# Performance work log

Measured on AMD Instinct MI355X. Metric: run time of the kernel, lower is better.

The kernel has to match this reference:

```python
import jax, jax.numpy as jnp
import numpy as np

B, L, A = 256, 512, 40          # proteins, residues per protein, atoms per drug
FD, FT, LD = 78, 54, 128        # drug feat, protein feat, latent dim
P = L + 1                       # residues + 1 appended drug super-node


def setup_inputs() -> dict:
    key = jax.random.key(0)
    ks = iter(jax.random.split(key, 48))
    Nd = B * A
    # drug graphs: chain bonds, both directions
    i = np.arange(A - 1)
    s = np.concatenate([i, i + 1]); d = np.concatenate([i + 1, i])
    off = (np.arange(B) * A)[:, None]
    drug_ei = jnp.asarray(np.stack([(s[None] + off).ravel(), (d[None] + off).ravel()]), jnp.int32)
    drug_batch = jnp.asarray(np.repeat(np.arange(B), A), jnp.int32)
    # protein graphs: residue chain + drug super-node (local idx L) connected to all residues in order
    r = np.arange(L - 1)
    ps = np.concatenate([r, r + 1, np.full(L, L), np.arange(L)])
    pd = np.concatenate([r + 1, r, np.arange(L), np.full(L, L)])
    poff = (np.arange(B) * P)[:, None]
    prot_ei = jnp.asarray(np.stack([(ps[None] + poff).ravel(), (pd[None] + poff).ravel()]), jnp.int32)
    prot_batch = jnp.asarray(np.repeat(np.arange(B), P), jnp.int32)
    E2 = B * (2 * (L - 1) + 2 * L)

    def lin(fi, fo):
        return jax.random.normal(next(ks), (fi, fo), jnp.float32) / np.float32(np.sqrt(fi))

    def vec(fo):
        return jnp.zeros((fo,), jnp.float32)

    return dict(
        drug_x=jax.random.normal(next(ks), (Nd, FD), jnp.float32),
        drug_ei=drug_ei, drug_batch=drug_batch,
        prot_x=jax.random.normal(next(ks), (B * P, FT), jnp.float32),
        prot_ei=prot_ei, prot_batch=prot_batch,
        prot_ea=jax.random.uniform(next(ks), (E2,), jnp.float32),
        W_c1d=lin(FD, FD), b_c1d=vec(FD),
        W_c2d=lin(FD, 2 * FD), b_c2d=vec(2 * FD),
        W_rd_g=lin(2 * FD, 2 * FD), b_rd_g=vec(2 * FD), W_rd_l=lin(2 * FD, 2 * FD),
        W_fg1d=lin(2 * FD, 1024), b_fg1d=vec(1024),
        W_fg2d=lin(1024, FT), b_fg2d=vec(FT),
        W_fg3d=lin(FT, 2 * LD), b_fg3d=vec(2 * LD),
        W_att1=lin(FT, FT), b_att1=vec(FT),
        W_att2=lin(FT, 1), b_att2=vec(1),
        W_c1t=lin(FT, LD), b_c1t=vec(LD),
        W_c2t=lin(LD, 2 * LD), b_c2t=vec(2 * LD),
        W_rt_g=lin(2 * LD, 2 * LD), b_rt_g=vec(2 * LD), W_rt_l=lin(2 * LD, 2 * LD),
        W_fg1t=lin(2 * LD, 1024), b_fg1t=vec(1024),
        W_fg2t=lin(1024, 2 * LD), b_fg2t=vec(2 * LD),
        W_fc1=lin(4 * LD, 1024), b_fc1=vec(1024),
        W_fc2=lin(1024, 512), b_fc2=vec(512),
        W_out=lin(512, 1), b_out=vec(1),
    )


def _gcn(x, W, b, src, dst, ew, n):
    # PyG GCNConv: symmetric norm with self-loops (fill value 1), optional edge weights
    h = x @ W
    deg = jax.ops.segment_sum(ew, dst, num_segments=n) + 1.0
    dinv = jax.lax.rsqrt(deg)
    norm = dinv[src] * ew * dinv[dst]
    agg = jax.ops.segment_sum(h[src] * norm[:, None], dst, num_segments=n)
    return agg + h * (dinv * dinv)[:, None] + b


def _rblock(x, Wg, bg, Wl, src, dst, ew, n):
    h = jax.nn.relu(_gcn(x, Wg, bg, src, dst, ew, n))
    return jax.nn.relu(h @ Wl + x)


def reference(drug_x, drug_ei, drug_batch, prot_x, prot_ei, prot_batch, prot_ea,
              W_c1d, b_c1d, W_c2d, b_c2d, W_rd_g, b_rd_g, W_rd_l,
              W_fg1d, b_fg1d, W_fg2d, b_fg2d, W_fg3d, b_fg3d,
              W_att1, b_att1, W_att2, b_att2,
              W_c1t, b_c1t, W_c2t, b_c2t, W_rt_g, b_rt_g, W_rt_l,
              W_fg1t, b_fg1t, W_fg2t, b_fg2t,
              W_fc1, b_fc1, W_fc2, b_fc2, W_out, b_out):
    relu = jax.nn.relu
    Nd, N2 = drug_x.shape[0], prot_x.shape[0]
    sd, dd = drug_ei[0], drug_ei[1]
    ewd = jnp.ones(sd.shape[0], drug_x.dtype)
    x = relu(_gcn(drug_x, W_c1d, b_c1d, sd, dd, ewd, Nd))
    x = relu(_gcn(x, W_c2d, b_c2d, sd, dd, ewd, Nd))
    for _ in range(4):  # shared-weight residual block applied num_rblock times
        x = _rblock(x, W_rd_g, b_rd_g, W_rd_l, sd, dd, ewd, Nd)
    xg = jax.ops.segment_max(x, drug_batch, num_segments=B)  # global max pool
    x = relu(xg @ W_fg1d + b_fg1d)
    x = x @ W_fg2d + b_fg2d                                   # [B, FT]
    x_chg = relu(x @ W_fg3d + b_fg3d)                          # [B, 2*LD]
    # vectorized per-protein attention (replaces the python loop over prot_lens)
    res = prot_x.reshape(B, P, FT)[:, :L]                      # residues only
    att = jnp.tanh(res @ W_att1 + b_att1) @ W_att2 + b_att2    # [B, L, 1]
    att = jax.nn.softmax(att[..., 0], axis=1)                  # [B, L]
    att_node = jnp.concatenate([att, jnp.zeros((B, 1), att.dtype)], 1).reshape(-1)
    drug_idx = (jnp.arange(B) + 1) * P - 1
    is_drug = jnp.zeros((N2,), bool).at[drug_idx].set(True)
    st, dt = prot_ei[0], prot_ei[1]
    # edges touching a drug super-node get that residue's attention weight
    ea = jnp.where(is_drug[st], att_node[dt], jnp.where(is_drug[dt], att_node[st], prot_ea))
    x2 = prot_x.at[drug_idx].set(x)                            # inject drug embeddings
    x2 = relu(_gcn(x2, W_c1t, b_c1t, st, dt, ea, N2))
    x2 = relu(_gcn(x2, W_c2t, b_c2t, st, dt, ea, N2))
    ew1 = jnp.ones(st.shape[0], x2.dtype)
    for _ in range(4):
        x2 = _rblock(x2, W_rt_g, b_rt_g, W_rt_l, st, dt, ew1, N2)
    x2r = x2.reshape(B, P, 2 * LD)
    x2g = x2r[:, :L].max(axis=1)                               # gmp over residues (drug node masked out)
    drug_after = x2r[:, L]
    x2v = relu(x2g @ W_fg1t + b_fg1t) @ W_fg2t + b_fg2t
    xm = jnp.maximum(drug_after, x_chg)                        # max_pool1d(kernel=2) over the pair
    xc = jnp.concatenate([xm, x2v], 1)
    xc = relu(xc @ W_fc1 + b_fc1)
    xc = relu(xc @ W_fc2 + b_fc2)
    return xc @ W_out + b_out
```

## Files before the change

### kernel.cpp

```cpp
#include <hip/hip_runtime.h>
#include <cstdio>

#define B_   256
#define L_   512
#define A_   40
#define FD_  78
#define FT_  54
#define LD_  128
#define P_   513
#define ND_  (B_*A_)
#define N2_  (B_*P_)
#define EB_  2046

typedef __attribute__((ext_vector_type(8))) short short8;
typedef __attribute__((ext_vector_type(4))) float floatx4;
typedef unsigned short u16;

__device__ __forceinline__ short f2bf(float f) {
    union { float f; unsigned u; } v; v.f = f;
    unsigned u = v.u;
    u += 0x7fff + ((u >> 16) & 1);
    return (short)(u >> 16);
}
__device__ __forceinline__ float bf2f(u16 s) {
    union { unsigned u; float f; } v; v.u = ((unsigned)s) << 16; return v.f;
}

#define TBK 32
#define LDK 40
#define CSP 260

#define SYNC_LDS asm volatile("s_waitcnt lgkmcnt(0)\n\ts_barrier" ::: "memory")

__global__ __launch_bounds__(256) void gemm_mfma_k(
    const float* __restrict__ A, const short* __restrict__ WT,
    float* __restrict__ C, int M, int N, int K, int Kp)
{
    __shared__ short As[128 * LDK];
    __shared__ short Bs[128 * LDK];
    const int bm = blockIdx.y * 128;
    const int bn = blockIdx.x * 128;
    const int tid  = threadIdx.x;
    const int wave = tid >> 6, lane = tid & 63;
    const int wm = (wave >> 1) * 64, wn = (wave & 1) * 64;
    const int lrow = lane & 15, quad = lane >> 4;

    floatx4 acc[4][4] = {};

    for (int k0 = 0; k0 < Kp; k0 += TBK) {
#pragma unroll
        for (int it = 0; it < 2; ++it) {
            int g   = it * 256 + tid;
            int row = g >> 2, kg = g & 3;
            int kb  = k0 + kg * 8;
            const float* arow = A + (size_t)(bm + row) * K + kb;
            short8 av;
#pragma unroll
            for (int j = 0; j < 8; ++j) av[j] = (kb + j < K) ? f2bf(arow[j]) : (short)0;
            *(short8*)&As[row * LDK + kg * 8] = av;
            *(short8*)&Bs[row * LDK + kg * 8] = *(const short8*)(WT + (size_t)(bn + row) * Kp + kb);
        }
        __syncthreads();
        short8 af[4], bfv[4];
#pragma unroll
        for (int i = 0; i < 4; ++i)
            af[i] = *(short8*)&As[(wm + i * 16 + lrow) * LDK + quad * 8];
#pragma unroll
        for (int j = 0; j < 4; ++j)
            bfv[j] = *(short8*)&Bs[(wn + j * 16 + lrow) * LDK + quad * 8];
#pragma unroll
        for (int i = 0; i < 4; ++i)
#pragma unroll
            for (int j = 0; j < 4; ++j)
                acc[i][j] = __builtin_amdgcn_mfma_f32_16x16x32_bf16(af[i], bfv[j], acc[i][j], 0, 0, 0);
        __syncthreads();
    }
#pragma unroll
    for (int i = 0; i < 4; ++i) {
        int grow0 = bm + wm + i * 16 + quad * 4;
#pragma unroll
        for (int j = 0; j < 4; ++j) {
            int col = bn + wn + j * 16 + lrow;
            size_t base = (size_t)grow0 * N + col;
#pragma unroll
            for (int r = 0; r < 4; ++r)
                C[base + (size_t)r * N] = acc[i][j][r];
        }
    }
}

__global__ __launch_bounds__(256) void gemm_bb_k(
    const u16* __restrict__ A, int lda, const short* __restrict__ WT, int Kp,
    const u16* __restrict__ resid, u16* __restrict__ C, int N, int act)
{
    __shared__ short As[128 * LDK];
    __shared__ short Bs[128 * LDK];
    const int bm = blockIdx.y * 128;
    const int bn = blockIdx.x * 128;
    const int tid  = threadIdx.x;
    const int wave = tid >> 6, lane = tid & 63;
    const int wm = (wave >> 1) * 64, wn = (wave & 1) * 64;
    const int lrow = lane & 15, quad = lane >> 4;

    floatx4 acc[4][4] = {};

    for (int k0 = 0; k0 < Kp; k0 += TBK) {
#pragma unroll
        for (int it = 0; it < 2; ++it) {
            int g   = it * 256 + tid;
            int row = g >> 2, kg = g & 3;
            int kb  = k0 + kg * 8;
            *(short8*)&As[row * LDK + kg * 8] = *(const short8*)(A + (size_t)(bm + row) * lda + kb);
            *(short8*)&Bs[row * LDK + kg * 8] = *(const short8*)(WT + (size_t)(bn + row) * Kp + kb);
        }
        __syncthreads();
        short8 af[4], bfv[4];
#pragma unroll
        for (int i = 0; i < 4; ++i)
            af[i] = *(short8*)&As[(wm + i * 16 + lrow) * LDK + quad * 8];
#pragma unroll
        for (int j = 0; j < 4; ++j)
            bfv[j] = *(short8*)&Bs[(wn + j * 16 + lrow) * LDK + quad * 8];
#pragma unroll
        for (int i = 0; i < 4; ++i)
#pragma unroll
            for (int j = 0; j < 4; ++j)
                acc[i][j] = __builtin_amdgcn_mfma_f32_16x16x32_bf16(af[i], bfv[j], acc[i][j], 0, 0, 0);
        __syncthreads();
    }
#pragma unroll
    for (int i = 0; i < 4; ++i) {
        int grow0 = bm + wm + i * 16 + quad * 4;
#pragma unroll
        for (int j = 0; j < 4; ++j) {
            int col = bn + wn + j * 16 + lrow;
            size_t base = (size_t)grow0 * N + col;
#pragma unroll
            for (int r = 0; r < 4; ++r) {
                float v = acc[i][j][r];
                size_t idx = base + (size_t)r * N;
                if (resid) v += bf2f(resid[idx]);
                if (act)   v = fmaxf(v, 0.f);
                C[idx] = (u16)f2bf(v);
            }
        }
    }
}

template<int KT>
__global__ __launch_bounds__(256, 2) void gemm_n256pw_k(
    const u16* __restrict__ A, const short* __restrict__ WT,
    const u16* __restrict__ resid, u16* __restrict__ C, int act,
    const float* __restrict__ cInF, float* __restrict__ Wacc)
{
    constexpr int K = KT * TBK;
    __shared__ short As[64 * LDK];
    __shared__ float Cs[16 * CSP];
    const int bm = blockIdx.x * 64;
    const int tid  = threadIdx.x;
    const int wave = tid >> 6, lane = tid & 63;
    const int wn = wave * 64;
    const int lrow = lane & 15, quad = lane >> 4;
    const int srow = tid >> 2, skg = tid & 3;

    floatx4 acc[4][4] = {};

    short8 aR[KT];
#pragma unroll
    for (int kt = 0; kt < KT; ++kt)
        aR[kt] = *(const short8*)(A + (size_t)(bm + srow) * K + kt * TBK + skg * 8);

    const short* bp0 = WT + (size_t)(wn +  0 + lrow) * K + quad * 8;
    const short* bp1 = WT + (size_t)(wn + 16 + lrow) * K + quad * 8;
    const short* bp2 = WT + (size_t)(wn + 32 + lrow) * K + quad * 8;
    const short* bp3 = WT + (size_t)(wn + 48 + lrow) * K + quad * 8;
    short8 bfv[2][4];
    bfv[0][0] = *(const short8*)bp0;
    bfv[0][1] = *(const short8*)bp1;
    bfv[0][2] = *(const short8*)bp2;
    bfv[0][3] = *(const short8*)bp3;

#pragma unroll
    for (int kt = 0; kt < KT; ++kt) {
        const int cur = kt & 1, nxt = cur ^ 1;
        *(short8*)&As[srow * LDK + skg * 8] = aR[kt];
        SYNC_LDS;
        if (kt + 1 < KT) {
            const int kn = (kt + 1) * TBK;
            bfv[nxt][0] = *(const short8*)(bp0 + kn);
            bfv[nxt][1] = *(const short8*)(bp1 + kn);
            bfv[nxt][2] = *(const short8*)(bp2 + kn);
            bfv[nxt][3] = *(const short8*)(bp3 + kn);
        }
        short8 af[4];
#pragma unroll
        for (int i = 0; i < 4; ++i)
            af[i] = *(short8*)&As[(i * 16 + lrow) * LDK + quad * 8];
#pragma unroll
        for (int i = 0; i < 4; ++i)
#pragma unroll
            for (int j = 0; j < 4; ++j)
                acc[i][j] = __builtin_amdgcn_mfma_f32_16x16x32_bf16(af[i], bfv[cur][j], acc[i][j], 0, 0, 0);
        SYNC_LDS;
    }

    if (cInF) {
        const int b0 = bm / P_;
        const int b1 = (bm + 63) / P_;
        float s0[4] = {0.f, 0.f, 0.f, 0.f};
        float s1[4] = {0.f, 0.f, 0.f, 0.f};
#pragma unroll
        for (int i = 0; i < 4; ++i) {
#pragma unroll
            for (int r = 0; r < 4; ++r) {
                int grow = bm + i * 16 + quad * 4 + r;
                float ci = cInF[grow];
                bool hi = (grow / P_) != b0;
#pragma unroll
                for (int j = 0; j < 4; ++j) {
                    float v = ci * acc[i][j][r];
                    if (hi) s1[j] += v; else s0[j] += v;
                }
            }
        }
#pragma unroll
        for (int j = 0; j < 4; ++j) {
            s0[j] += __shfl_xor(s0[j], 16);
            s0[j] += __shfl_xor(s0[j], 32);
            s1[j] += __shfl_xor(s1[j], 16);
            s1[j] += __shfl_xor(s1[j], 32);
        }
        if (quad == 0) {
#pragma unroll
            for (int j = 0; j < 4; ++j) {
                int col = wn + j * 16 + lrow;
                atomicAdd(&Wacc[(size_t)b0 * 256 + col], s0[j]);
                if (b1 != b0) atomicAdd(&Wacc[(size_t)b1 * 256 + col], s1[j]);
            }
        }
    }

    const int erl = tid >> 4;
    const int ecc = (tid & 15) * 16;
#pragma unroll
    for (int i = 0; i < 4; ++i) {
#pragma unroll
        for (int j = 0; j < 4; ++j)
#pragma unroll
            for (int r = 0; r < 4; ++r)
                Cs[(quad * 4 + r) * CSP + wn + j * 16 + lrow] = acc[i][j][r];
        SYNC_LDS;
        const int grow = bm + i * 16 + erl;
        const size_t gbase = (size_t)grow * 256 + ecc;
#pragma unroll
        for (int h = 0; h < 2; ++h) {
            const float* cp = &Cs[erl * CSP + ecc + h * 8];
            short8 ov;
            if (resid) {
                short8 rv = *(const short8*)(resid + gbase + h * 8);
#pragma unroll
                for (int e = 0; e < 8; ++e) {
                    float v = cp[e] + bf2f((u16)rv[e]);
                    if (act) v = fmaxf(v, 0.f);
                    ov[e] = f2bf(v);
                }
            } else {
#pragma unroll
                for (int e = 0; e < 8; ++e) {
                    float v = cp[e];
                    if (act) v = fmaxf(v, 0.f);
                    ov[e] = f2bf(v);
                }
            }
            *(short8*)(C + gbase + h * 8) = ov;
        }
        SYNC_LDS;
    }
}

template<int KT>
__global__ __launch_bounds__(256, 2) void gemm_aggl_k(
    const u16* __restrict__ U, const short* __restrict__ WT,
    const float* __restrict__ cPc, const float* __restrict__ cNc,
    const float* __restrict__ cDc, const float* __restrict__ cSc,
    const float* __restrict__ Wacc, const float* __restrict__ bias,
    const u16* __restrict__ resid, u16* __restrict__ C)
{
    constexpr int K = KT * TBK;
    __shared__ short As[64 * LDK];
    __shared__ float Cs[16 * CSP];
    const int bm = blockIdx.x * 64;
    const int tid  = threadIdx.x;
    const int wave = tid >> 6, lane = tid & 63;
    const int wn = wave * 64;
    const int lrow = lane & 15, quad = lane >> 4;
    const int srow = tid >> 2, skg = tid & 3;

    const int r    = bm + srow;
    const int bl   = r / P_;
    const int irow = r - bl * P_;
    const bool isD = (irow == L_);
    const size_t rD = (size_t)bl * P_ + L_;
    const int rm = (r == 0) ? 0 : r - 1;
    const int rp = (r == N2_ - 1) ? r : r + 1;
    const float cs = cSc[r];
    const float cp = isD ? 0.f : cPc[r];
    const float cn = isD ? 0.f : cNc[r];
    const float cd = isD ? 0.f : cDc[r];
    const float* wrow = Wacc + (size_t)bl * 256;

    floatx4 acc[4][4] = {};

    const u16* uSp = U + (size_t)r  * K + skg * 8;
    const u16* uMp = U + (size_t)rm * K + skg * 8;
    const u16* uPp = U + (size_t)rp * K + skg * 8;
    const u16* uDp = U + rD * K + skg * 8;

    short8 uS[KT];
#pragma unroll
    for (int kt = 0; kt < KT; ++kt) uS[kt] = *(const short8*)(uSp + kt * TBK);
    short8 uM = *(const short8*)uMp;
    short8 uP = *(const short8*)uPp;
    short8 uD = *(const short8*)uDp;

    const short* bp0 = WT + (size_t)(wn +  0 + lrow) * K + quad * 8;
    const short* bp1 = WT + (size_t)(wn + 16 + lrow) * K + quad * 8;
    const short* bp2 = WT + (size_t)(wn + 32 + lrow) * K + quad * 8;
    const short* bp3 = WT + (size_t)(wn + 48 + lrow) * K + quad * 8;

#pragma unroll
    for (int kt = 0; kt < KT; ++kt) {
        const int kb = kt * TBK + skg * 8;
        float4 bi0 = *(const float4*)(bias + kb);
        float4 bi1 = *(const float4*)(bias + kb + 4);
        float bv[8] = {bi0.x, bi0.y, bi0.z, bi0.w, bi1.x, bi1.y, bi1.z, bi1.w};
        if (isD) {
            float4 w0 = *(const float4*)(wrow + kb);
            float4 w1 = *(const float4*)(wrow + kb + 4);
            bv[0] += w0.x; bv[1] += w0.y; bv[2] += w0.z; bv[3] += w0.w;
            bv[4] += w1.x; bv[5] += w1.y; bv[6] += w1.z; bv[7] += w1.w;
        }
        short8 av;
#pragma unroll
        for (int e = 0; e < 8; ++e) {
            float v = cs * bf2f((u16)uS[kt][e]) + cp * bf2f((u16)uM[e])
                    + cn * bf2f((u16)uP[e]) + cd * bf2f((u16)uD[e]) + bv[e];
            av[e] = f2bf(fmaxf(v, 0.f));
        }
        *(short8*)&As[srow * LDK + skg * 8] = av;
        const int kc = kt * TBK;
        short8 bfv0 = *(const short8*)(bp0 + kc);
        short8 bfv1 = *(const short8*)(bp1 + kc);
        short8 bfv2 = *(const short8*)(bp2 + kc);
        short8 bfv3 = *(const short8*)(bp3 + kc);
        SYNC_LDS;
        if (kt + 1 < KT) {
            const int kn = (kt + 1) * TBK;
            uM = *(const short8*)(uMp + kn);
            uP = *(const short8*)(uPp + kn);
            uD = *(const short8*)(uDp + kn);
        }
        short8 af[4];
#pragma unroll
        for (int i = 0; i < 4; ++i)
            af[i] = *(short8*)&As[(i * 16 + lrow) * LDK + quad * 8];
#pragma unroll
        for (int i = 0; i < 4; ++i) {
            acc[i][0] = __builtin_amdgcn_mfma_f32_16x16x32_bf16(af[i], bfv0, acc[i][0], 0, 0, 0);
            acc[i][1] = __builtin_amdgcn_mfma_f32_16x16x32_bf16(af[i], bfv1, acc[i][1], 0, 0, 0);
            acc[i][2] = __builtin_amdgcn_mfma_f32_16x16x32_bf16(af[i], bfv2, acc[i][2], 0, 0, 0);
            acc[i][3] = __builtin_amdgcn_mfma_f32_16x16x32_bf16(af[i], bfv3, acc[i][3], 0, 0, 0);
        }
        SYNC_LDS;
    }

    const int erl = tid >> 4;
    const int ecc = (tid & 15) * 16;
#pragma unroll
    for (int i = 0; i < 4; ++i) {
#pragma unroll
        for (int j = 0; j < 4; ++j)
#pragma unroll
            for (int r2 = 0; r2 < 4; ++r2)
                Cs[(quad * 4 + r2) * CSP + wn + j * 16 + lrow] = acc[i][j][r2];
        SYNC_LDS;
        const int grow = bm + i * 16 + erl;
        const size_t gbase = (size_t)grow * 256 + ecc;
#pragma unroll
        for (int h = 0; h < 2; ++h) {
            const float* cp2 = &Cs[erl * CSP + ecc + h * 8];
            short8 rv = *(const short8*)(resid + gbase + h * 8);
            short8 ov;
#pragma unroll
            for (int e = 0; e < 8; ++e) {
                float v = cp2[e] + bf2f((u16)rv[e]);
                ov[e] = f2bf(fmaxf(v, 0.f));
            }
            *(short8*)(C + gbase + h * 8) = ov;
        }
        SYNC_LDS;
    }
}

static inline void gemm_n256(const u16* A, int K, const short* WT,
                             const u16* resid, u16* C, int act,
                             const float* cInF, float* Wacc, hipStream_t s)
{
    dim3 g(N2_ / 64), b(256);
    if (K == 128)
        hipLaunchKernelGGL((gemm_n256pw_k<4>), g, b, 0, s, A, WT, resid, C, act, cInF, Wacc);
    else
        hipLaunchKernelGGL((gemm_n256pw_k<8>), g, b, 0, s, A, WT, resid, C, act, cInF, Wacc);
}

__global__ void wt_cvt_k(const float* __restrict__ W, short* __restrict__ WT,
                         int K, int Nreal, int Kp, int Ntot)
{
    int idx = blockIdx.x * 256 + threadIdx.x;
    if (idx >= Ntot * Kp) return;
    int n = idx / Kp, k = idx - n * Kp;
    WT[idx] = (k < K && n < Nreal) ? f2bf(W[(size_t)k * Nreal + n]) : (short)0;
}

#define BM 64
#define BN 64
#define BKK 16
__global__ __launch_bounds__(256) void gemm_k(
    const float* __restrict__ Amat, const float* __restrict__ Wmat,
    const float* __restrict__ bias, const float* __restrict__ resid,
    float* __restrict__ Cmat, int M, int N, int K, int act)
{
    __shared__ float As[BKK][BM + 4];
    __shared__ float Ws[BKK][BN];
    const int bm = blockIdx.y * BM;
    const int bn = blockIdx.x * BN;
    const int tx = threadIdx.x, ty = threadIdx.y;
    const int tid = ty * 16 + tx;
    float acc[4][4] = {};

    for (int k0 = 0; k0 < K; k0 += BKK) {
#pragma unroll
        for (int j = 0; j < 4; ++j) {
            int l = tid + 256 * j;
            int m = l >> 4, kk = l & 15;
            int gm = bm + m, gk = k0 + kk;
            As[kk][m] = (gm < M && gk < K) ? Amat[(size_t)gm * K + gk] : 0.f;
        }
#pragma unroll
        for (int j = 0; j < 4; ++j) {
            int l = tid + 256 * j;
            int kk = l >> 6, n = l & 63;
            int gk = k0 + kk, gn = bn + n;
            Ws[kk][n] = (gk < K && gn < N) ? Wmat[(size_t)gk * N + gn] : 0.f;
        }
        __syncthreads();
#pragma unroll
        for (int k = 0; k < BKK; ++k) {
            float4 a4 = *(const float4*)&As[k][ty * 4];
            float4 w4 = *(const float4*)&Ws[k][tx * 4];
            float av[4] = {a4.x, a4.y, a4.z, a4.w};
            float wv[4] = {w4.x, w4.y, w4.z, w4.w};
#pragma unroll
            for (int i = 0; i < 4; ++i)
#pragma unroll
                for (int j = 0; j < 4; ++j)
                    acc[i][j] = fmaf(av[i], wv[j], acc[i][j]);
        }
        __syncthreads();
    }
#pragma unroll
    for (int i = 0; i < 4; ++i) {
        int gm = bm + ty * 4 + i;
        if (gm >= M) continue;
#pragma unroll
        for (int j = 0; j < 4; ++j) {
            int gn = bn + tx * 4 + j;
            if (gn >= N) continue;
            float v = acc[i][j];
            if (bias)  v += bias[gn];
            if (resid) v += resid[(size_t)gm * N + gn];
            if (act)   v = fmaxf(v, 0.f);
            Cmat[(size_t)gm * N + gn] = v;
        }
    }
}

static inline void gemm(const float* A, const float* W, const float* bias,
                        const float* resid, float* C, int M, int N, int K, int act,
                        hipStream_t s)
{
    dim3 g((N + BN - 1) / BN, (M + BM - 1) / BM), b(16, 16);
    hipLaunchKernelGGL(gemm_k, g, b, 0, s, A, W, bias, resid, C, M, N, K, act);
}

__global__ __launch_bounds__(256) void gemm_skA_k(
    const float* __restrict__ Amat, const float* __restrict__ Wmat,
    float* __restrict__ part, int M, int N, int K, int Kc)
{
    __shared__ float As[BKK][BM + 4];
    __shared__ float Ws[BKK][BN];
    const int bm = blockIdx.y * BM;
    const int bn = blockIdx.x * BN;
    const int sk = blockIdx.z;
    const int kb0  = sk * Kc;
    const int kend = min(K, kb0 + Kc);
    const int tx = threadIdx.x, ty = threadIdx.y;
    const int tid = ty * 16 + tx;
    float acc[4][4] = {};

    for (int k0 = kb0; k0 < kend; k0 += BKK) {
#pragma unroll
        for (int j = 0; j < 4; ++j) {
            int l = tid + 256 * j;
            int m = l >> 4, kk = l & 15;
            int gm = bm + m, gk = k0 + kk;
            As[kk][m] = (gm < M && gk < kend) ? Amat[(size_t)gm * K + gk] : 0.f;
        }
#pragma unroll
        for (int j = 0; j < 4; ++j) {
            int l = tid + 256 * j;
            int kk = l >> 6, n = l & 63;
            int gk = k0 + kk, gn = bn + n;
            Ws[kk][n] = (gk < kend && gn < N) ? Wmat[(size_t)gk * N + gn] : 0.f;
        }
        __syncthreads();
#pragma unroll
        for (int k = 0; k < BKK; ++k) {
            float4 a4 = *(const float4*)&As[k][ty * 4];
            float4 w4 = *(const float4*)&Ws[k][tx * 4];
            float av[4] = {a4.x, a4.y, a4.z, a4.w};
            float wv[4] = {w4.x, w4.y, w4.z, w4.w};
#pragma unroll
            for (int i = 0; i < 4; ++i)
#pragma unroll
                for (int j = 0; j < 4; ++j)
                    acc[i][j] = fmaf(av[i], wv[j], acc[i][j]);
        }
        __syncthreads();
    }
#pragma unroll
    for (int i = 0; i < 4; ++i) {
        int gm = bm + ty * 4 + i;
        if (gm >= M) continue;
#pragma unroll
        for (int j = 0; j < 4; ++j) {
            int gn = bn + tx * 4 + j;
            if (gn >= N) continue;
            part[((size_t)sk * M + gm) * N + gn] = acc[i][j];
        }
    }
}

__global__ void gemm_skB_k(const float* __restrict__ part, const float* __restrict__ bias,
                           float* __restrict__ C, int M, int N, int SK, int act)
{
    int idx = blockIdx.x * 256 + threadIdx.x;
    if (idx >= M * N) return;
    int n = idx % N;
    float v = bias ? bias[n] : 0.f;
    for (int s = 0; s < SK; ++s) v += part[(size_t)s * M * N + idx];
    if (act) v = fmaxf(v, 0.f);
    C[idx] = v;
}

static inline void gemm_sk(const float* A, const float* W, const float* bias,
                           float* C, float* skbuf, int M, int N, int K, int SK, int act,
                           hipStream_t s)
{
    int Kc = (K + SK - 1) / SK;
    dim3 g((N + 63) / 64, (M + 63) / 64, SK), b(16, 16);
    hipLaunchKernelGGL(gemm_skA_k, g, b, 0, s, A, W, skbuf, M, N, K, Kc);
    hipLaunchKernelGGL(gemm_skB_k, dim3((M * N + 255) / 256), dim3(256), 0, s,
                       skbuf, bias, C, M, N, SK, act);
}

__global__ void drug_agg_k(const float* __restrict__ h, const float* __restrict__ bias,
                           float* __restrict__ out, int F)
{
    int r = blockIdx.x;
    int a = r % A_;
    int t = threadIdx.x;
    if (t >= F) return;
    const float DI2 = 0.70710678118654752f;
    const float DI3 = 0.57735026918962576f;
    float da = (a == 0 || a == A_ - 1) ? DI2 : DI3;
    const float* hs = h + (size_t)r * F;
    float v = da * da * hs[t] + bias[t];
    if (a > 0) {
        float dp = (a - 1 == 0) ? DI2 : DI3;
        v += dp * da * hs[t - F];
    }
    if (a < A_ - 1) {
        float dn = (a + 1 == A_ - 1) ? DI2 : DI3;
        v += dn * da * hs[t + F];
    }
    out[(size_t)r * F + t] = fmaxf(v, 0.f);
}

__global__ void drug_max_k(const float* __restrict__ x, float* __restrict__ xg)
{
    int b = blockIdx.x, t = threadIdx.x;
    if (t >= 2 * FD_) return;
    const float* xb = x + (size_t)b * A_ * (2 * FD_);
    float m = -INFINITY;
    for (int a = 0; a < A_; ++a) m = fmaxf(m, xb[a * (2 * FD_) + t]);
    xg[b * (2 * FD_) + t] = m;
}

__global__ __launch_bounds__(256) void att_dot_k(
    const float* __restrict__ Hs, const float* __restrict__ b1,
    const float* __restrict__ W2, const float* __restrict__ b2,
    float* __restrict__ scores)
{
    int w = threadIdx.x >> 6, lane = threadIdx.x & 63;
    float b1v = (lane < FT_) ? b1[lane] : 0.f;
    float w2v = (lane < FT_) ? W2[lane] : 0.f;
    float b2v = b2[0];
    int base = blockIdx.x * 64 + w * 16;
    for (int rr = 0; rr < 16; ++rr) {
        int r = base + rr;
        float v = 0.f;
        if (lane < FT_) v = tanhf(Hs[(size_t)r * 128 + lane] + b1v) * w2v;
#pragma unroll
        for (int o = 32; o; o >>= 1) v += __shfl_down(v, o);
        if (lane == 0) {
            int bl = r / P_, i = r - bl * P_;
            if (i < L_) scores[bl * L_ + i] = v + b2v;
        }
    }
}

__global__ __launch_bounds__(512) void softmax_k(
    const float* __restrict__ scores, float* __restrict__ att, float* __restrict__ attsum)
{
    int b = blockIdx.x, t = threadIdx.x;
    __shared__ float sm[8];
    __shared__ float bcast;
    float v = scores[b * L_ + t];
    float m = v;
#pragma unroll
    for (int o = 32; o; o >>= 1) m = fmaxf(m, __shfl_down(m, o));
    if ((t & 63) == 0) sm[t >> 6] = m;
    __syncthreads();
    if (t == 0) { float mm = sm[0]; for (int i = 1; i < 8; ++i) mm = fmaxf(mm, sm[i]); bcast = mm; }
    __syncthreads();
    float mx = bcast;
    float e = expf(v - mx);
    float s = e;
#pragma unroll
    for (int o = 32; o; o >>= 1) s += __shfl_down(s, o);
    __syncthreads();
    if ((t & 63) == 0) sm[t >> 6] = s;
    __syncthreads();
    if (t == 0) { float ss = 0; for (int i = 0; i < 8; ++i) ss += sm[i]; bcast = ss; }
    __syncthreads();
    float a = e / bcast;
    att[b * L_ + t] = a;
    float s2 = a;
#pragma unroll
    for (int o = 32; o; o >>= 1) s2 += __shfl_down(s2, o);
    __syncthreads();
    if ((t & 63) == 0) sm[t >> 6] = s2;
    __syncthreads();
    if (t == 0) { float ss = 0; for (int i = 0; i < 8; ++i) ss += sm[i]; attsum[b] = ss; }
}

__global__ void coef_deg_k(const float* __restrict__ prot_ea, const float* __restrict__ att,
                           const float* __restrict__ attsum, float* __restrict__ dinv, int use_ea)
{
    int r = blockIdx.x * 256 + threadIdx.x;
    if (r >= N2_) return;
    int b = r / P_, i = r - b * P_;
    float deg;
    if (i == L_) {
        deg = 1.f + (use_ea ? attsum[b] : (float)L_);
    } else {
        float wP = (i >= 1)      ? (use_ea ? prot_ea[b * EB_ + (i - 1)]   : 1.f) : 0.f;
        float wN = (i <= L_ - 2) ? (use_ea ? prot_ea[b * EB_ + 511 + i]   : 1.f) : 0.f;
        float wD = use_ea ? att[b * L_ + i] : 1.f;
        deg = 1.f + wP + wN + wD;
    }
    dinv[r] = rsqrtf(deg);
}

__global__ void coef_k(const float* __restrict__ dinv, const float* __restrict__ prot_ea,
                       const float* __restrict__ att, float* __restrict__ cP, float* __restrict__ cN,
                       float* __restrict__ cD, float* __restrict__ cS, float* __restrict__ cIn,
                       float* __restrict__ cInF, int use_ea)
{
    int r = blockIdx.x * 256 + threadIdx.x;
    if (r >= N2_) return;
    int b = r / P_, i = r - b * P_;
    float di = dinv[r];
    cS[r] = di * di;
    if (i == L_) { cP[r] = 0.f; cN[r] = 0.f; cD[r] = 0.f; cInF[r] = 0.f; return; }
    float wP = (i >= 1)      ? (use_ea ? prot_ea[b * EB_ + (i - 1)] : 1.f) : 0.f;
    float wN = (i <= L_ - 2) ? (use_ea ? prot_ea[b * EB_ + 511 + i] : 1.f) : 0.f;
    float wD = use_ea ? att[b * L_ + i] : 1.f;
    float dD = dinv[b * P_ + L_];
    cP[r] = (i >= 1)      ? dinv[r - 1] * wP * di : 0.f;
    cN[r] = (i <= L_ - 2) ? dinv[r + 1] * wN * di : 0.f;
    cD[r] = dD * wD * di;
    float ci = di * wD * dD;
    cIn[b * L_ + i] = ci;
    cInF[r] = ci;
}

template<int F>
__global__ __launch_bounds__(256) void prot_agg_res_k(
    const u16* __restrict__ h, const float* __restrict__ cP,
    const float* __restrict__ cN, const float* __restrict__ cD,
    const float* __restrict__ cS, const float* __restrict__ cIn,
    const float* __restrict__ bias, u16* __restrict__ outp,
    float* __restrict__ Wacc)
{
    constexpr int G = F / 8;
    constexpr int RPB = 256 / G;
    __shared__ float pacc[RPB * F];
    int t = threadIdx.x;
    int rl = t / G, g = t - rl * G;
    int base = blockIdx.x * RPB;
    int r = base + rl;
    int bl = r / P_, i = r - bl * P_;
    int f0 = g * 8;
    const u16* hs = h + (size_t)r * F + f0;
    if (i == L_) {
#pragma unroll
        for (int e = 0; e < 8; ++e) pacc[rl * F + f0 + e] = 0.f;
    } else {
        const u16* hd = h + ((size_t)bl * P_ + L_) * F + f0;
        float cs = cS[r], cd = cD[r], cp = cP[r], cn = cN[r];
        float ci = cIn[bl * L_ + i];
        short8 vs = *(const short8*)hs;
        short8 vd = *(const short8*)hd;
        short8 vp = *(const short8*)(hs - (i > 0 ? F : 0));
        short8 vn = *(const short8*)(hs + F);
        short8 ov;
#pragma unroll
        for (int e = 0; e < 8; ++e) {
            float hv = bf2f((u16)vs[e]);
            pacc[rl * F + f0 + e] = ci * hv;
            float v = cs * hv + cd * bf2f((u16)vd[e]) + bias[f0 + e];
            v += cp * bf2f((u16)vp[e]);
            v += cn * bf2f((u16)vn[e]);
            ov[e] = f2bf(fmaxf(v, 0.f));
        }
        *(short8*)(outp + (size_t)r * F + f0) = ov;
    }
    __syncthreads();
    int f = t;
    if (f < F) {
        int b0   = base / P_;
        int bend = (base + RPB - 1) / P_;
        float s0 = 0.f, s1 = 0.f;
#pragma unroll
        for (int rr = 0; rr < RPB; ++rr) {
            float v = pacc[rr * F + f];
            if ((base + rr) / P_ == b0) s0 += v; else s1 += v;
        }
        atomicAdd(&Wacc[(size_t)b0 * F + f], s0);
        if (bend != b0) atomicAdd(&Wacc[(size_t)bend * F + f], s1);
    }
}

__global__ void drug_fin_k(const float* __restrict__ Wacc, const u16* __restrict__ h,
                           const float* __restrict__ cS, const float* __restrict__ bias,
                           u16* __restrict__ outp, int F)
{
    int bl = blockIdx.x, t = threadIdx.x;
    if (t >= F) return;
    size_t rD = (size_t)bl * P_ + L_;
    float v = Wacc[(size_t)bl * F + t] + cS[rD] * bf2f(h[rD * F + t]) + bias[t];
    outp[rD * F + t] = (u16)f2bf(fmaxf(v, 0.f));
}

__global__ void xin_k(const float* __restrict__ prot_x, const float* __restrict__ t2d,
                      u16* __restrict__ Xin)
{
    int idx = blockIdx.x * 256 + threadIdx.x;
    if (idx >= N2_ * 64) return;
    int r = idx >> 6, t = idx & 63;
    int bl = r / P_, i = r - bl * P_;
    float v = 0.f;
    if (t < FT_) v = (i == L_) ? t2d[bl * FT_ + t] : prot_x[(size_t)r * FT_ + t];
    Xin[idx] = (u16)f2bf(v);
}

__global__ __launch_bounds__(256) void x2g_bf2_k(const u16* __restrict__ X,
                                                 float* __restrict__ x2g, float* __restrict__ da)
{
    __shared__ float red[2048];
    int t = threadIdx.x;
    int rl = t >> 5, g = t & 31;
    int bl = blockIdx.x, f0 = g * 8;
    const u16* xb = X + (size_t)bl * P_ * 256;
    float m[8];
#pragma unroll
    for (int e = 0; e < 8; ++e) m[e] = -INFINITY;
    for (int j = rl; j < L_; j += 8) {
        short8 v = *(const short8*)(xb + (size_t)j * 256 + f0);
#pragma unroll
        for (int e = 0; e < 8; ++e) m[e] = fmaxf(m[e], bf2f((u16)v[e]));
    }
#pragma unroll
    for (int e = 0; e < 8; ++e) red[rl * 256 + f0 + e] = m[e];
    __syncthreads();
    if (rl == 0) {
        short8 vd = *(const short8*)(xb + (size_t)L_ * 256 + f0);
#pragma unroll
        for (int e = 0; e < 8; ++e) {
            float v = red[f0 + e];
            for (int rr = 1; rr < 8; ++rr) v = fmaxf(v, red[rr * 256 + f0 + e]);
            x2g[bl * 256 + f0 + e] = v;
            da[bl * 256 + f0 + e] = bf2f((u16)vd[e]);
        }
    }
}

__global__ void build_xc_k(const float* __restrict__ da, const float* __restrict__ x_chg,
                           const float* __restrict__ x2v, float* __restrict__ xc)
{
    int idx = blockIdx.x * 256 + threadIdx.x;
    if (idx >= B_ * 512) return;
    int b = idx >> 9, c = idx & 511;
    float v = (c < 256) ? fmaxf(da[b * 256 + c], x_chg[b * 256 + c])
                        : x2v[b * 256 + (c - 256)];
    xc[idx] = v;
}

__global__ __launch_bounds__(64) void out_k(const float* __restrict__ f2,
                                            const float* __restrict__ W,
                                            const float* __restrict__ bias,
                                            float* __restrict__ out)
{
    int row = blockIdx.x, t = threadIdx.x;
    float v = 0.f;
    for (int k = t; k < 512; k += 64) v = fmaf(f2[(size_t)row * 512 + k], W[k], v);
#pragma unroll
    for (int o = 32; o; o >>= 1) v += __shfl_down(v, o);
    if (t == 0) out[row] = v + bias[0];
}

extern "C" void kernel_launch(void* const* d_in, const int* in_sizes, int n_in,
                              void* d_out, int out_size, void* d_ws, size_t ws_size,
                              hipStream_t stream)
{
    const float* drug_x  = (const float*)d_in[0];
    const float* prot_x  = (const float*)d_in[3];
    const float* prot_ea = (const float*)d_in[6];
    const float* W_c1d = (const float*)d_in[7];   const float* b_c1d = (const float*)d_in[8];
    const float* W_c2d = (const float*)d_in[9];   const float* b_c2d = (const float*)d_in[10];
    const float* W_rd_g = (const float*)d_in[11]; const float* b_rd_g = (const float*)d_in[12];
    const float* W_rd_l = (const float*)d_in[13];
    const float* W_fg1d = (const float*)d_in[14]; const float* b_fg1d = (const float*)d_in[15];
    const float* W_fg2d = (const float*)d_in[16]; const float* b_fg2d = (const float*)d_in[17];
    const float* W_fg3d = (const float*)d_in[18]; const float* b_fg3d = (const float*)d_in[19];
    const float* W_att1 = (const float*)d_in[20]; const float* b_att1 = (const float*)d_in[21];
    const float* W_att2 = (const float*)d_in[22]; const float* b_att2 = (const float*)d_in[23];
    const float* W_c1t = (const float*)d_in[24];  const float* b_c1t = (const float*)d_in[25];
    const float* W_c2t = (const float*)d_in[26];  const float* b_c2t = (const float*)d_in[27];
    const float* W_rt_g = (const float*)d_in[28]; const float* b_rt_g = (const float*)d_in[29];
    const float* W_rt_l = (const float*)d_in[30];
    const float* W_fg1t = (const float*)d_in[31]; const float* b_fg1t = (const float*)d_in[32];
    const float* W_fg2t = (const float*)d_in[33]; const float* b_fg2t = (const float*)d_in[34];
    const float* W_fc1 = (const float*)d_in[35];  const float* b_fc1 = (const float*)d_in[36];
    const float* W_fc2 = (const float*)d_in[37];  const float* b_fc2 = (const float*)d_in[38];
    const float* W_out = (const float*)d_in[39];  const float* b_out = (const float*)d_in[40];
    float* out = (float*)d_out;

    float* ws = (float*)d_ws;
    size_t off = 0;
    auto alloc = [&](size_t n) {
        n = (n + 3) & ~(size_t)3;
        float* p = ws + off; off += n; return p;
    };

    u16* U = (u16*)alloc((size_t)N2_ * 128);
    u16* V = (u16*)alloc((size_t)N2_ * 128);
    u16* X = (u16*)alloc((size_t)N2_ * 128);
    u16* Xin = (u16*)alloc((size_t)N2_ * 32);
    float* Hs = (float*)U;
    float* Wacc = alloc(B_ * 256);
    float* dA = alloc((size_t)ND_ * 156);
    float* dB = alloc((size_t)ND_ * 156);
    float* dC = alloc((size_t)ND_ * 156);
    float* xg    = alloc(B_ * 156);
    float* t1d   = alloc(B_ * 1024);
    float* t2d   = alloc(B_ * FT_);
    float* x_chg = alloc(B_ * 256);
    float* scores = alloc(B_ * 512);
    float* att    = alloc(B_ * 512);
    float* attsum = alloc(B_);
    float* dinvE = alloc(N2_);
    float* cPE = alloc(N2_); float* cNE = alloc(N2_); float* cDE = alloc(N2_); float* cSE = alloc(N2_);
    float* cInE = alloc(B_ * 512);
    float* cInFE = alloc(N2_);
    float* dinvO = alloc(N2_);
    float* cPO = alloc(N2_); float* cNO = alloc(N2_); float* cDO = alloc(N2_); float* cSO = alloc(N2_);
    float* cInO = alloc(B_ * 512);
    float* cInFO = alloc(N2_);
    float* x2g = alloc(B_ * 256);
    float* dafter = alloc(B_ * 256);
    float* t1t = alloc(B_ * 1024);
    float* x2v = alloc(B_ * 256);
    float* xc  = alloc(B_ * 512);
    float* f1  = alloc(B_ * 1024);
    float* f2  = alloc(B_ * 512);
    float* skbuf = alloc((size_t)2 * 1024 * 1024);
    short* WT_c1t = (short*)alloc(128 * 64 / 2);
    short* WT_c2t = (short*)alloc(256 * 128 / 2);
    short* WT_rtg = (short*)alloc(256 * 256 / 2);
    short* WT_rtl = (short*)alloc(256 * 256 / 2);
    short* WT_att = (short*)alloc(128 * 64 / 2);

    if (off * sizeof(float) > ws_size) {
        fprintf(stderr, "kernel_launch: workspace too small: need %zu, have %zu\n",
                off * sizeof(float), ws_size);
        return;
    }

    hipLaunchKernelGGL(wt_cvt_k, dim3((128 * 64 + 255) / 256), dim3(256), 0, stream,  W_c1t, WT_c1t, FT_, 128, 64, 128);
    hipLaunchKernelGGL(wt_cvt_k, dim3((256 * 128 + 255) / 256), dim3(256), 0, stream, W_c2t, WT_c2t, 128, 256, 128, 256);
    hipLaunchKernelGGL(wt_cvt_k, dim3((256 * 256 + 255) / 256), dim3(256), 0, stream, W_rt_g, WT_rtg, 256, 256, 256, 256);
    hipLaunchKernelGGL(wt_cvt_k, dim3((256 * 256 + 255) / 256), dim3(256), 0, stream, W_rt_l, WT_rtl, 256, 256, 256, 256);
    hipLaunchKernelGGL(wt_cvt_k, dim3((128 * 64 + 255) / 256), dim3(256), 0, stream,  W_att1, WT_att, FT_, FT_, 64, 128);

    gemm(drug_x, W_c1d, nullptr, nullptr, dB, ND_, FD_, FD_, 0, stream);
    hipLaunchKernelGGL(drug_agg_k, dim3(ND_), dim3(128), 0, stream, dB, b_c1d, dA, FD_);
    gemm(dA, W_c2d, nullptr, nullptr, dB, ND_, 2 * FD_, FD_, 0, stream);
    hipLaunchKernelGGL(drug_agg_k, dim3(ND_), dim3(192), 0, stream, dB, b_c2d, dA, 2 * FD_);
    for (int it = 0; it < 4; ++it) {
        gemm(dA, W_rd_g, nullptr, nullptr, dB, ND_, 2 * FD_, 2 * FD_, 0, stream);
        hipLaunchKernelGGL(drug_agg_k, dim3(ND_), dim3(192), 0, stream, dB, b_rd_g, dC, 2 * FD_);
        gemm(dC, W_rd_l, nullptr, dA, dB, ND_, 2 * FD_, 2 * FD_, 1, stream);
        float* tmp = dA; dA = dB; dB = tmp;
    }
    hipLaunchKernelGGL(drug_max_k, dim3(B_), dim3(192), 0, stream, dA, xg);
    gemm_sk(xg,  W_fg1d, b_fg1d, t1d,   skbuf, B_, 1024, 156, 4, 1, stream);
    gemm_sk(t1d, W_fg2d, b_fg2d, t2d,   skbuf, B_, FT_, 1024, 16, 0, stream);
    gemm_sk(t2d, W_fg3d, b_fg3d, x_chg, skbuf, B_, 2 * LD_, FT_, 2, 1, stream);

    {
        dim3 g(1, N2_ / 128), b(256);
        hipLaunchKernelGGL(gemm_mfma_k, g, b, 0, stream, prot_x, WT_att, Hs, N2_, 128, FT_, 64);
    }
    hipLaunchKernelGGL(att_dot_k, dim3(N2_ / 64), dim3(256), 0, stream, Hs, b_att1, W_att2, b_att2, scores);
    hipLaunchKernelGGL(softmax_k, dim3(B_), dim3(512), 0, stream, scores, att, attsum);

    hipLaunchKernelGGL(coef_deg_k, dim3((N2_ + 255) / 256), dim3(256), 0, stream, prot_ea, att, attsum, dinvE, 1);
    hipLaunchKernelGGL(coef_k, dim3((N2_ + 255) / 256), dim3(256), 0, stream, dinvE, prot_ea, att, cPE, cNE, cDE, cSE, cInE, cInFE, 1);
    hipLaunchKernelGGL(coef_deg_k, dim3((N2_ + 255) / 256), dim3(256), 0, stream, prot_ea, att, attsum, dinvO, 0);
    hipLaunchKernelGGL(coef_k, dim3((N2_ + 255) / 256), dim3(256), 0, stream, dinvO, prot_ea, att, cPO, cNO, cDO, cSO, cInO, cInFO, 0);

    hipLaunchKernelGGL(xin_k, dim3((N2_ * 64 + 255) / 256), dim3(256), 0, stream, prot_x, t2d, Xin);

    {
        dim3 g(1, N2_ / 128), b(256);
        hipLaunchKernelGGL(gemm_bb_k, g, b, 0, stream, Xin, 64, WT_c1t, 64,
                           (const u16*)nullptr, U, 128, 0);
    }
    hipMemsetAsync(Wacc, 0, B_ * 128 * sizeof(float), stream);
    hipLaunchKernelGGL((prot_agg_res_k<128>), dim3(N2_ / 16), dim3(256), 0, stream,
                       U, cPE, cNE, cDE, cSE, cInE, b_c1t, V, Wacc);
    hipLaunchKernelGGL(drug_fin_k, dim3(B_), dim3(128), 0, stream, Wacc, U, cSE, b_c1t, V, 128);
    gemm_n256(V, 128, WT_c2t, (const u16*)nullptr, U, 0, nullptr, nullptr, stream);
    hipMemsetAsync(Wacc, 0, B_ * 256 * sizeof(float), stream);
    hipLaunchKernelGGL((prot_agg_res_k<256>), dim3(N2_ / 8), dim3(256), 0, stream,
                       U, cPE, cNE, cDE, cSE, cInE, b_c2t, X, Wacc);
    hipLaunchKernelGGL(drug_fin_k, dim3(B_), dim3(256), 0, stream, Wacc, U, cSE, b_c2t, X, 256);

    for (int it = 0; it < 4; ++it) {
        hipMemsetAsync(Wacc, 0, B_ * 256 * sizeof(float), stream);
        gemm_n256(X, 256, WT_rtg, (const u16*)nullptr, U, 0, cInFO, Wacc, stream);
        {
            dim3 g(N2_ / 64), b(256);
            hipLaunchKernelGGL((gemm_aggl_k<8>), g, b, 0, stream,
                               U, WT_rtl, cPO, cNO, cDO, cSO, Wacc, b_rt_g, X, X);
        }
    }

    hipLaunchKernelGGL(x2g_bf2_k, dim3(B_), dim3(256), 0, stream, X, x2g, dafter);

    gemm_sk(x2g, W_fg1t, b_fg1t, t1t, skbuf, B_, 1024, 256, 8, 1, stream);
    gemm_sk(t1t, W_fg2t, b_fg2t, x2v, skbuf, B_, 256, 1024, 16, 0, stream);
    hipLaunchKernelGGL(build_xc_k, dim3(B_ * 512 / 256), dim3(256), 0, stream, dafter, x_chg, x2v, xc);
    gemm_sk(xc, W_fc1, b_fc1, f1, skbuf, B_, 1024, 512, 8, 1, stream);
    gemm_sk(f1, W_fc2, b_fc2, f2, skbuf, B_, 512, 1024, 16, 1, stream);
    hipLaunchKernelGGL(out_k, dim3(B_), dim3(64), 0, stream, f2, W_out, b_out, out);
}
```

Baseline: 1.315 ms.

## Fuse entire drug GCN branch into one per-graph kernel with LDS-resident features

Replaces the chain of drug-branch launches (one small GEMM plus one aggregation kernel per layer, four residual blocks, and a max-pool) with one kernel that runs one block per drug graph. Each block keeps its 40-atom feature matrix in LDS. Each thread computes one output column over all 40 atoms in registers, applies the chain-graph normalisation in-register, and finishes with the max-pool. This removes about twenty launches and the global round-trips of intermediate activations. In exchange, only 256 blocks run with many idle threads (at most 156 of 256 active), and per-thread register pressure is high (80 floats), which may limit occupancy.

```diff
diff --git a/kernel.cpp b/kernel.cpp
--- a/kernel.cpp
+++ b/kernel.cpp
@@ -31,6 +31,113 @@
 #define CSP 260
 
 #define SYNC_LDS asm volatile("s_waitcnt lgkmcnt(0)\n\ts_barrier" ::: "memory")
+
+__global__ __launch_bounds__(256) void drug_fused_k(
+    const float* __restrict__ drug_x,
+    const float* __restrict__ W_c1d, const float* __restrict__ b_c1d,
+    const float* __restrict__ W_c2d, const float* __restrict__ b_c2d,
+    const float* __restrict__ W_rd_g, const float* __restrict__ b_rd_g,
+    const float* __restrict__ W_rd_l,
+    float* __restrict__ xg)
+{
+    __shared__ float Xb[2][156 * 40];
+    const int b = blockIdx.x, t = threadIdx.x;
+    const float DI2 = 0.70710678118654752f;
+    const float DI3 = 0.57735026918962576f;
+
+    for (int idx = t; idx < 40 * 78; idx += 256) {
+        int r = idx / 78, k = idx - r * 78;
+        Xb[0][k * 40 + r] = drug_x[(size_t)(b * A_ + r) * FD_ + k];
+    }
+    __syncthreads();
+
+    float acc[40], hn[40];
+
+#define DCOL_GEMM(Wp, K, N, SRC)                                        \
+    {                                                                   \
+        _Pragma("unroll")                                               \
+        for (int r = 0; r < 40; ++r) acc[r] = 0.f;                      \
+        if (t < (N)) {                                                  \
+            for (int k = 0; k < (K); ++k) {                             \
+                float w = (Wp)[(size_t)k * (N) + t];                    \
+                const float* xp = &Xb[SRC][k * 40];                     \
+                _Pragma("unroll")                                       \
+                for (int r = 0; r < 40; ++r)                            \
+                    acc[r] = fmaf(xp[r], w, acc[r]);                    \
+            }                                                           \
+        }                                                               \
+    }
+
+#define DCOL_AGG(BIASV)                                                 \
+    {                                                                   \
+        _Pragma("unroll")                                               \
+        for (int r = 0; r < 40; ++r) {                                  \
+            float da = (r == 0 || r == A_ - 1) ? DI2 : DI3;             \
+            float v = da * da * acc[r] + (BIASV);                       \
+            if (r > 0)                                                  \
+                v += ((r - 1 == 0) ? DI2 : DI3) * da * acc[r - 1];      \
+            if (r < A_ - 1)                                             \
+                v += ((r + 1 == A_ - 1) ? DI2 : DI3) * da * acc[r + 1]; \
+            hn[r] = fmaxf(v, 0.f);                                      \
+        }                                                               \
+    }
+
+    DCOL_GEMM(W_c1d, FD_, FD_, 0);
+    {
+        float bi = (t < FD_) ? b_c1d[t] : 0.f;
+        DCOL_AGG(bi);
+        if (t < FD_) {
+#pragma unroll
+            for (int r = 0; r < 40; ++r) Xb[1][t * 40 + r] = hn[r];
+        }
+    }
+    __syncthreads();
+
+    DCOL_GEMM(W_c2d, FD_, 2 * FD_, 1);
+    {
+        float bi = (t < 2 * FD_) ? b_c2d[t] : 0.f;
+        DCOL_AGG(bi);
+        if (t < 2 * FD_) {
+#pragma unroll
+            for (int r = 0; r < 40; ++r) Xb[0][t * 40 + r] = hn[r];
+        }
+    }
+    __syncthreads();
+
+    for (int it = 0; it < 4; ++it) {
+        DCOL_GEMM(W_rd_g, 2 * FD_, 2 * FD_, 0);
+        {
+            float bi = (t < 2 * FD_) ? b_rd_g[t] : 0.f;
+            DCOL_AGG(bi);
+            if (t < 2 * FD_) {
+#pragma unroll
+                for (int r = 0; r < 40; ++r) Xb[1][t * 40 + r] = hn[r];
+            }
+        }
+        __syncthreads();
+        DCOL_GEMM(W_rd_l, 2 * FD_, 2 * FD_, 1);
+        if (t < 2 * FD_) {
+#pragma unroll
+            for (int r = 0; r < 40; ++r)
+                hn[r] = fmaxf(acc[r] + Xb[0][t * 40 + r], 0.f);
+        }
+        __syncthreads();
+        if (t < 2 * FD_) {
+#pragma unroll
+            for (int r = 0; r < 40; ++r) Xb[0][t * 40 + r] = hn[r];
+        }
+        __syncthreads();
+    }
+
+    if (t < 2 * FD_) {
+        float m = -INFINITY;
+#pragma unroll
+        for (int r = 0; r < 40; ++r) m = fmaxf(m, Xb[0][t * 40 + r]);
+        xg[(size_t)b * (2 * FD_) + t] = m;
+    }
+#undef DCOL_GEMM
+#undef DCOL_AGG
+}
 
 __global__ __launch_bounds__(256) void gemm_mfma_k(
     const float* __restrict__ A, const short* __restrict__ WT,
@@ -425,74 +532,6 @@
 #define BM 64
 #define BN 64
 #define BKK 16
-__global__ __launch_bounds__(256) void gemm_k(
-    const float* __restrict__ Amat, const float* __restrict__ Wmat,
-    const float* __restrict__ bias, const float* __restrict__ resid,
-    float* __restrict__ Cmat, int M, int N, int K, int act)
-{
-    __shared__ float As[BKK][BM + 4];
-    __shared__ float Ws[BKK][BN];
-    const int bm = blockIdx.y * BM;
-    const int bn = blockIdx.x * BN;
-    const int tx = threadIdx.x, ty = threadIdx.y;
-    const int tid = ty * 16 + tx;
-    float acc[4][4] = {};
-
-    for (int k0 = 0; k0 < K; k0 += BKK) {
-#pragma unroll
-        for (int j = 0; j < 4; ++j) {
-            int l = tid + 256 * j;
-            int m = l >> 4, kk = l & 15;
-            int gm = bm + m, gk = k0 + kk;
-            As[kk][m] = (gm < M && gk < K) ? Amat[(size_t)gm * K + gk] : 0.f;
-        }
-#pragma unroll
-        for (int j = 0; j < 4; ++j) {
-            int l = tid + 256 * j;
-            int kk = l >> 6, n = l & 63;
-            int gk = k0 + kk, gn = bn + n;
-            Ws[kk][n] = (gk < K && gn < N) ? Wmat[(size_t)gk * N + gn] : 0.f;
-        }
-        __syncthreads();
-#pragma unroll
-        for (int k = 0; k < BKK; ++k) {
-            float4 a4 = *(const float4*)&As[k][ty * 4];
-            float4 w4 = *(const float4*)&Ws[k][tx * 4];
-            float av[4] = {a4.x, a4.y, a4.z, a4.w};
-            float wv[4] = {w4.x, w4.y, w4.z, w4.w};
-#pragma unroll
-            for (int i = 0; i < 4; ++i)
-#pragma unroll
-                for (int j = 0; j < 4; ++j)
-                    acc[i][j] = fmaf(av[i], wv[j], acc[i][j]);
-        }
-        __syncthreads();
-    }
-#pragma unroll
-    for (int i = 0; i < 4; ++i) {
-        int gm = bm + ty * 4 + i;
-        if (gm >= M) continue;
-#pragma unroll
-        for (int j = 0; j < 4; ++j) {
-            int gn = bn + tx * 4 + j;
-            if (gn >= N) continue;
-            float v = acc[i][j];
-            if (bias)  v += bias[gn];
-            if (resid) v += resid[(size_t)gm * N + gn];
-            if (act)   v = fmaxf(v, 0.f);
-            Cmat[(size_t)gm * N + gn] = v;
-        }
-    }
-}
-
-static inline void gemm(const float* A, const float* W, const float* bias,
-                        const float* resid, float* C, int M, int N, int K, int act,
-                        hipStream_t s)
-{
-    dim3 g((N + BN - 1) / BN, (M + BM - 1) / BM), b(16, 16);
-    hipLaunchKernelGGL(gemm_k, g, b, 0, s, A, W, bias, resid, C, M, N, K, act);
-}
-
 __global__ __launch_bounds__(256) void gemm_skA_k(
     const float* __restrict__ Amat, const float* __restrict__ Wmat,
     float* __restrict__ part, int M, int N, int K, int Kc)
@@ -572,39 +611,6 @@
     hipLaunchKernelGGL(gemm_skA_k, g, b, 0, s, A, W, skbuf, M, N, K, Kc);
     hipLaunchKernelGGL(gemm_skB_k, dim3((M * N + 255) / 256), dim3(256), 0, s,
                        skbuf, bias, C, M, N, SK, act);
-}
-
-__global__ void drug_agg_k(const float* __restrict__ h, const float* __restrict__ bias,
-                           float* __restrict__ out, int F)
-{
-    int r = blockIdx.x;
-    int a = r % A_;
-    int t = threadIdx.x;
-    if (t >= F) return;
-    const float DI2 = 0.70710678118654752f;
-    const float DI3 = 0.57735026918962576f;
-    float da = (a == 0 || a == A_ - 1) ? DI2 : DI3;
-    const float* hs = h + (size_t)r * F;
-    float v = da * da * hs[t] + bias[t];
-    if (a > 0) {
-        float dp = (a - 1 == 0) ? DI2 : DI3;
-        v += dp * da * hs[t - F];
-    }
-    if (a < A_ - 1) {
-        float dn = (a + 1 == A_ - 1) ? DI2 : DI3;
-        v += dn * da * hs[t + F];
-    }
-    out[(size_t)r * F + t] = fmaxf(v, 0.f);
-}
-
-__global__ void drug_max_k(const float* __restrict__ x, float* __restrict__ xg)
-{
-    int b = blockIdx.x, t = threadIdx.x;
-    if (t >= 2 * FD_) return;
-    const float* xb = x + (size_t)b * A_ * (2 * FD_);
-    float m = -INFINITY;
-    for (int a = 0; a < A_; ++a) m = fmaxf(m, xb[a * (2 * FD_) + t]);
-    xg[b * (2 * FD_) + t] = m;
 }
 
 __global__ __launch_bounds__(256) void att_dot_k(
@@ -881,9 +887,6 @@
     u16* Xin = (u16*)alloc((size_t)N2_ * 32);
     float* Hs = (float*)U;
     float* Wacc = alloc(B_ * 256);
-    float* dA = alloc((size_t)ND_ * 156);
-    float* dB = alloc((size_t)ND_ * 156);
-    float* dC = alloc((size_t)ND_ * 156);
     float* xg    = alloc(B_ * 156);
     float* t1d   = alloc(B_ * 1024);
     float* t2d   = alloc(B_ * FT_);
@@ -925,17 +928,8 @@
     hipLaunchKernelGGL(wt_cvt_k, dim3((256 * 256 + 255) / 256), dim3(256), 0, stream, W_rt_l, WT_rtl, 256, 256, 256, 256);
     hipLaunchKernelGGL(wt_cvt_k, dim3((128 * 64 + 255) / 256), dim3(256), 0, stream,  W_att1, WT_att, FT_, FT_, 64, 128);
 
-    gemm(drug_x, W_c1d, nullptr, nullptr, dB, ND_, FD_, FD_, 0, stream);
-    hipLaunchKernelGGL(drug_agg_k, dim3(ND_), dim3(128), 0, stream, dB, b_c1d, dA, FD_);
-    gemm(dA, W_c2d, nullptr, nullptr, dB, ND_, 2 * FD_, FD_, 0, stream);
-    hipLaunchKernelGGL(drug_agg_k, dim3(ND_), dim3(192), 0, stream, dB, b_c2d, dA, 2 * FD_);
-    for (int it = 0; it < 4; ++it) {
-        gemm(dA, W_rd_g, nullptr, nullptr, dB, ND_, 2 * FD_, 2 * FD_, 0, stream);
-        hipLaunchKernelGGL(drug_agg_k, dim3(ND_), dim3(192), 0, stream, dB, b_rd_g, dC, 2 * FD_);
-        gemm(dC, W_rd_l, nullptr, dA, dB, ND_, 2 * FD_, 2 * FD_, 1, stream);
-        float* tmp = dA; dA = dB; dB = tmp;
-    }
-    hipLaunchKernelGGL(drug_max_k, dim3(B_), dim3(192), 0, stream, dA, xg);
+    hipLaunchKernelGGL(drug_fused_k, dim3(B_), dim3(256), 0, stream,
+                       drug_x, W_c1d, b_c1d, W_c2d, b_c2d, W_rd_g, b_rd_g, W_rd_l, xg);
     gemm_sk(xg,  W_fg1d, b_fg1d, t1d,   skbuf, B_, 1024, 156, 4, 1, stream);
     gemm_sk(t1d, W_fg2d, b_fg2d, t2d,   skbuf, B_, FT_, 1024, 16, 0, stream);
     gemm_sk(t2d, W_fg3d, b_fg3d, x_chg, skbuf, B_, 2 * LD_, FT_, 2, 1, stream);
```

New measurement: 1.193 ms. 1.1x faster.
